# Optimization experiments

Measured on AMD Instinct MI355X. Metric: run time of the kernel, lower is better.

Reference implementation:

```python
import jax, jax.numpy as jnp
import numpy as np

EPS = 1e-12  # matches torch F.normalize default eps

def setup_inputs() -> dict:
    key = jax.random.key(0)
    k1, k2 = jax.random.split(key)
    x_pred = jax.random.normal(k1, (4, 4, 64, 64), dtype=jnp.float32)
    x_src = jax.random.normal(k2, (4, 4, 64, 64), dtype=jnp.float32)
    return {"x_pred": x_pred, "x_src": x_src}

def _l2_normalize_channels(z):
    # z: [B, C, N]; normalize along C (torch F.normalize: x / max(||x||, eps))
    norm = jnp.sqrt(jnp.sum(z * z, axis=1, keepdims=True))
    return z / jnp.maximum(norm, EPS)

def reference(x_pred, x_src):
    x_pred = x_pred.astype(jnp.float32)
    x_src = x_src.astype(jnp.float32)
    B, C, H, W = x_pred.shape
    N = H * W
    z_pred = _l2_normalize_channels(x_pred.reshape(B, C, N))
    z_src = _l2_normalize_channels(x_src.reshape(B, C, N))
    # Gram matrices: [B, N, N] cosine similarity between spatial positions
    A_pred = jnp.einsum('bcn,bcm->bnm', z_pred, z_pred)
    A_src = jnp.einsum('bcn,bcm->bnm', z_src, z_src)
    diff = A_pred - A_src
    loss = jnp.sum(diff * diff)
    loss = loss / (B * N * N)
    return loss
```

## Files before the change

### kernel.cpp

```cpp
#include <hip/hip_runtime.h>
#include <math.h>


#define NORM_EPS 1e-12f

__global__ __launch_bounds__(64) void cosine_ssm_partial(
    const float* __restrict__ x_pred,
    const float* __restrict__ x_src,
    float* __restrict__ ws)
{
    constexpr int C = 4, N = 4096;
    const int slot = blockIdx.x;
    const int b    = slot >> 4;
    const int s    = slot & 15;
    const int lane = threadIdx.x;

    const float* pb = x_pred + (size_t)b * C * N;
    const float* sb = x_src  + (size_t)b * C * N;
    const int n0 = s * 256 + lane * 4;

    float pv[4][4], sv[4][4];
#pragma unroll
    for (int c = 0; c < C; ++c) {
        float4 t = *(const float4*)(pb + c * N + n0);
        pv[c][0] = t.x; pv[c][1] = t.y; pv[c][2] = t.z; pv[c][3] = t.w;
        float4 q = *(const float4*)(sb + c * N + n0);
        sv[c][0] = q.x; sv[c][1] = q.y; sv[c][2] = q.z; sv[c][3] = q.w;
    }

    float acc[36];
#pragma unroll
    for (int i = 0; i < 36; ++i) acc[i] = 0.f;

#pragma unroll
    for (int k = 0; k < 4; ++k) {
        float np = 0.f, ns = 0.f;
#pragma unroll
        for (int c = 0; c < 4; ++c) {
            np += pv[c][k] * pv[c][k];
            ns += sv[c][k] * sv[c][k];
        }
        const float ip = 1.f / fmaxf(sqrtf(np), NORM_EPS);
        const float is = 1.f / fmaxf(sqrtf(ns), NORM_EPS);
        float u[4], v[4];
#pragma unroll
        for (int c = 0; c < 4; ++c) { u[c] = pv[c][k] * ip; v[c] = sv[c][k] * is; }

        int idx = 0;
#pragma unroll
        for (int i = 0; i < 4; ++i)
#pragma unroll
            for (int j = i; j < 4; ++j) {
                acc[idx]      += u[i] * u[j];
                acc[10 + idx] += v[i] * v[j];
                ++idx;
            }
#pragma unroll
        for (int i = 0; i < 4; ++i)
#pragma unroll
            for (int j = 0; j < 4; ++j)
                acc[20 + i * 4 + j] += u[i] * v[j];
    }

#pragma unroll
    for (int off = 32; off >= 1; off >>= 1) {
#pragma unroll
        for (int i = 0; i < 36; ++i)
            acc[i] += __shfl_down(acc[i], off, 64);
    }

    if (lane == 0) {
#pragma unroll
        for (int i = 0; i < 36; ++i)
            ws[i * 64 + slot] = acc[i];
    }
}

__global__ __launch_bounds__(192) void cosine_ssm_finalize(
    const float* __restrict__ ws,
    float* __restrict__ out)
{
    __shared__ float g[4][36];
    __shared__ float contrib[4];
    const int t = threadIdx.x;

    if (t < 144) {
        const int b = t / 36;
        const int i = t - b * 36;
        const float* src = ws + i * 64 + b * 16;
        float ssum = 0.f;
#pragma unroll
        for (int s = 0; s < 16; ++s) ssum += src[s];
        g[b][i] = ssum;
    }
    __syncthreads();

    if (t < 4) {
        const float* a = g[t];
        const float fu = a[0]*a[0] + a[4]*a[4] + a[7]*a[7] + a[9]*a[9]
                       + 2.f*(a[1]*a[1] + a[2]*a[2] + a[3]*a[3] + a[5]*a[5] + a[6]*a[6] + a[8]*a[8]);
        const float* h = a + 10;
        const float fv = h[0]*h[0] + h[4]*h[4] + h[7]*h[7] + h[9]*h[9]
                       + 2.f*(h[1]*h[1] + h[2]*h[2] + h[3]*h[3] + h[5]*h[5] + h[6]*h[6] + h[8]*h[8]);
        const float* mm = a + 20;
        float fm = 0.f;
#pragma unroll
        for (int i = 0; i < 16; ++i) fm += mm[i] * mm[i];
        contrib[t] = fu + fv - 2.f * fm;
    }
    __syncthreads();

    if (t == 0) {
        const float scale = 1.0f / (4.0f * 4096.0f * 4096.0f);
        out[0] = (contrib[0] + contrib[1] + contrib[2] + contrib[3]) * scale;
    }
}

extern "C" void kernel_launch(void* const* d_in, const int* in_sizes, int n_in,
                              void* d_out, int out_size, void* d_ws, size_t ws_size,
                              hipStream_t stream) {
    const float* x_pred = (const float*)d_in[0];
    const float* x_src  = (const float*)d_in[1];
    float* ws  = (float*)d_ws;
    float* out = (float*)d_out;

    cosine_ssm_partial<<<64, 64, 0, stream>>>(x_pred, x_src, ws);
    cosine_ssm_finalize<<<1, 192, 0, stream>>>(ws, out);
}
```

Before: 59.54 us.

## Fuse partial and finalize kernels via cooperative grid sync

Merges the partial-Gram and finalize kernels into one cooperative kernel launched with 16 blocks of 256 threads. Each block reduces its four waves through LDS, writes partials to the workspace, then waits on a grid-wide sync so block 0 can compute the final loss. This removes one kernel launch and shrinks the cross-block reduction. In exchange it adds the cost of a cooperative launch and a grid barrier, and depends on cooperative launch being supported.

```diff
diff --git a/kernel.cpp b/kernel.cpp
--- a/kernel.cpp
+++ b/kernel.cpp
@@ -1,23 +1,29 @@
 #include <hip/hip_runtime.h>
+#include <hip/hip_cooperative_groups.h>
 #include <math.h>
 
 
+namespace cg = cooperative_groups;
+
 #define NORM_EPS 1e-12f
 
-__global__ __launch_bounds__(64) void cosine_ssm_partial(
+__global__ __launch_bounds__(256) void cosine_ssm_fused(
     const float* __restrict__ x_pred,
     const float* __restrict__ x_src,
-    float* __restrict__ ws)
+    float* __restrict__ ws,
+    float* __restrict__ out)
 {
     constexpr int C = 4, N = 4096;
     const int slot = blockIdx.x;
-    const int b    = slot >> 4;
-    const int s    = slot & 15;
-    const int lane = threadIdx.x;
+    const int b    = slot >> 2;
+    const int s    = slot & 3;
+    const int tid  = threadIdx.x;
+    const int lane = tid & 63;
+    const int wave = tid >> 6;
 
     const float* pb = x_pred + (size_t)b * C * N;
     const float* sb = x_src  + (size_t)b * C * N;
-    const int n0 = s * 256 + lane * 4;
+    const int n0 = s * 1024 + tid * 4;
 
     float pv[4][4], sv[4][4];
 #pragma unroll
@@ -69,50 +75,53 @@
             acc[i] += __shfl_down(acc[i], off, 64);
     }
 
+    __shared__ float lds[4][36];
     if (lane == 0) {
 #pragma unroll
-        for (int i = 0; i < 36; ++i)
-            ws[i * 64 + slot] = acc[i];
-    }
-}
-
-__global__ __launch_bounds__(192) void cosine_ssm_finalize(
-    const float* __restrict__ ws,
-    float* __restrict__ out)
-{
-    __shared__ float g[4][36];
-    __shared__ float contrib[4];
-    const int t = threadIdx.x;
-
-    if (t < 144) {
-        const int b = t / 36;
-        const int i = t - b * 36;
-        const float* src = ws + i * 64 + b * 16;
-        float ssum = 0.f;
-#pragma unroll
-        for (int s = 0; s < 16; ++s) ssum += src[s];
-        g[b][i] = ssum;
+        for (int i = 0; i < 36; ++i) lds[wave][i] = acc[i];
     }
     __syncthreads();
 
-    if (t < 4) {
-        const float* a = g[t];
-        const float fu = a[0]*a[0] + a[4]*a[4] + a[7]*a[7] + a[9]*a[9]
-                       + 2.f*(a[1]*a[1] + a[2]*a[2] + a[3]*a[3] + a[5]*a[5] + a[6]*a[6] + a[8]*a[8]);
-        const float* h = a + 10;
-        const float fv = h[0]*h[0] + h[4]*h[4] + h[7]*h[7] + h[9]*h[9]
-                       + 2.f*(h[1]*h[1] + h[2]*h[2] + h[3]*h[3] + h[5]*h[5] + h[6]*h[6] + h[8]*h[8]);
-        const float* mm = a + 20;
-        float fm = 0.f;
+    if (tid < 36) {
+        const float v0 = lds[0][tid] + lds[1][tid];
+        const float v1 = lds[2][tid] + lds[3][tid];
+        ws[tid * 16 + slot] = v0 + v1;
+    }
+    __threadfence();
+    cg::this_grid().sync();
+
+    if (blockIdx.x == 0) {
+        __shared__ float g[4][36];
+        __shared__ float contrib[4];
+        const int t = tid;
+
+        if (t < 144) {
+            const int bb = t / 36;
+            const int i  = t - bb * 36;
+            const float* src = ws + i * 16 + bb * 4;
+            g[bb][i] = (src[0] + src[1]) + (src[2] + src[3]);
+        }
+        __syncthreads();
+
+        if (t < 4) {
+            const float* a = g[t];
+            const float fu = a[0]*a[0] + a[4]*a[4] + a[7]*a[7] + a[9]*a[9]
+                           + 2.f*(a[1]*a[1] + a[2]*a[2] + a[3]*a[3] + a[5]*a[5] + a[6]*a[6] + a[8]*a[8]);
+            const float* h = a + 10;
+            const float fv = h[0]*h[0] + h[4]*h[4] + h[7]*h[7] + h[9]*h[9]
+                           + 2.f*(h[1]*h[1] + h[2]*h[2] + h[3]*h[3] + h[5]*h[5] + h[6]*h[6] + h[8]*h[8]);
+            const float* mm = a + 20;
+            float fm = 0.f;
 #pragma unroll
-        for (int i = 0; i < 16; ++i) fm += mm[i] * mm[i];
-        contrib[t] = fu + fv - 2.f * fm;
-    }
-    __syncthreads();
+            for (int i = 0; i < 16; ++i) fm += mm[i] * mm[i];
+            contrib[t] = fu + fv - 2.f * fm;
+        }
+        __syncthreads();
 
-    if (t == 0) {
-        const float scale = 1.0f / (4.0f * 4096.0f * 4096.0f);
-        out[0] = (contrib[0] + contrib[1] + contrib[2] + contrib[3]) * scale;
+        if (t == 0) {
+            const float scale = 1.0f / (4.0f * 4096.0f * 4096.0f);
+            out[0] = ((contrib[0] + contrib[1]) + (contrib[2] + contrib[3])) * scale;
+        }
     }
 }
 
@@ -124,6 +133,7 @@
     float* ws  = (float*)d_ws;
     float* out = (float*)d_out;
 
-    cosine_ssm_partial<<<64, 64, 0, stream>>>(x_pred, x_src, ws);
-    cosine_ssm_finalize<<<1, 192, 0, stream>>>(ws, out);
+    void* args[] = {(void*)&x_pred, (void*)&x_src, (void*)&ws, (void*)&out};
+    hipLaunchCooperativeKernel((void*)cosine_ssm_fused, dim3(16), dim3(256),
+                               args, 0, stream);
 }
```

Result: slower. 85.10 us (+42.9%).
